# Kernel tuning notes

Hardware: AMD Instinct MI355X
Metric: run time of the kernel (lower is better)

Reference implementation:

```python
import jax, jax.numpy as jnp
import numpy as np

# Module constants (from init_kwargs / derived)
KH, KW = 3, 3
STRIDE = (1, 1)
PAD = (1, 1)
DIL = (1, 1)
N_OFFSET_GRPS = 8  # offset.shape[1] // (2*KH*KW) = 144 // 18
N_WEIGHT_GRPS = 1


def setup_inputs() -> dict:
    key = jax.random.key(0)
    k1, k2, k3, k4, k5 = jax.random.split(key, 5)
    B, C, H, W = 4, 64, 128, 128
    inp = {
        "input": jax.random.normal(k1, (B, C, H, W), dtype=jnp.float32),
        "offset": jax.random.normal(k2, (B, 2 * N_OFFSET_GRPS * KH * KW, H, W), dtype=jnp.float32),
        "mask": jax.random.uniform(k3, (B, N_OFFSET_GRPS * KH * KW, H, W), dtype=jnp.float32),
        "weight": jax.random.normal(k4, (64, C, KH, KW), dtype=jnp.float32) * 0.05,
        "bias": jax.random.normal(k5, (64,), dtype=jnp.float32) * 0.05,
    }
    return inp


def _deform_conv2d(x, offset, mask, weight, bias):
    B, C, H, W = x.shape
    Ho, Wo = offset.shape[2], offset.shape[3]
    G = N_OFFSET_GRPS
    K = KH * KW
    Cg = C // G

    # base (un-deformed) sampling positions per kernel tap and output pixel
    ky, kx = jnp.meshgrid(jnp.arange(KH), jnp.arange(KW), indexing="ij")
    ky = ky.reshape(K)
    kx = kx.reshape(K)
    oy = jnp.arange(Ho) * STRIDE[0] - PAD[0]
    ox = jnp.arange(Wo) * STRIDE[1] - PAD[1]
    base_y = (oy[None, :, None] + (ky * DIL[0])[:, None, None]).astype(x.dtype)  # [K,Ho,1]
    base_x = (ox[None, None, :] + (kx * DIL[1])[:, None, None]).astype(x.dtype)  # [K,1,Wo]

    off = offset.reshape(B, G, K, 2, Ho, Wo)  # [...,0]=dy, [...,1]=dx
    py = base_y[None, None] + off[:, :, :, 0]  # [B,G,K,Ho,Wo]
    px = base_x[None, None] + off[:, :, :, 1]

    y0 = jnp.floor(py)
    x0 = jnp.floor(px)
    ly = py - y0  # fractional parts
    lx = px - x0
    y0i = y0.astype(jnp.int32)
    x0i = x0.astype(jnp.int32)

    xg = x.reshape(B, G, Cg, H * W)  # per-offset-group channel slices

    def corner(yi, xi):
        valid = ((yi >= 0) & (yi < H) & (xi >= 0) & (xi < W)).astype(x.dtype)
        idx = jnp.clip(yi, 0, H - 1) * W + jnp.clip(xi, 0, W - 1)  # [B,G,K,Ho,Wo]
        gather = lambda xbg, ibg: xbg[:, ibg]  # [Cg,H*W],[K,Ho,Wo] -> [Cg,K,Ho,Wo]
        v = jax.vmap(jax.vmap(gather))(xg, idx)  # [B,G,Cg,K,Ho,Wo]
        return v * valid[:, :, None]

    w00 = (1 - ly) * (1 - lx)
    w01 = (1 - ly) * lx
    w10 = ly * (1 - lx)
    w11 = ly * lx
    samp = (corner(y0i, x0i) * w00[:, :, None]
            + corner(y0i, x0i + 1) * w01[:, :, None]
            + corner(y0i + 1, x0i) * w10[:, :, None]
            + corner(y0i + 1, x0i + 1) * w11[:, :, None])  # [B,G,Cg,K,Ho,Wo]

    samp = samp * mask.reshape(B, G, 1, K, Ho, Wo)  # DCNv2 modulation
    col = samp.reshape(B, C, K, Ho, Wo)
    wr = weight.reshape(weight.shape[0], C, K)  # groups == 1
    out = jnp.einsum("ock,bckhw->bohw", wr, col) + bias[None, :, None, None]
    return out


def reference(input, offset, mask, weight, bias):
    return _deform_conv2d(input, offset, mask, weight, bias)
```

## Files before the change

kernel.cpp:

```cpp
#include <hip/hip_runtime.h>

#define HH 128
#define WW 128
#define CC 64
#define CO 64
#define BB 4
#define GG 8
#define CG 8
#define KK 9
#define HW (HH*WW)
#define PXT 16
#define NC 3
#define FRAG 512
#define NPOS (GG*KK*PXT)

typedef __attribute__((ext_vector_type(8))) short short8;
typedef __attribute__((ext_vector_type(4))) float floatx4;

union S8I { short8 s; int i[4]; };

__device__ inline short f2bf(float f) {
    union { float f; unsigned u; } v; v.f = f;
    return (short)((v.u + 0x7FFF + ((v.u >> 16) & 1)) >> 16);
}
__device__ inline unsigned rnd_bf(float f) {
    union { float f; unsigned u; } v; v.f = f;
    return v.u + 0x7FFF + ((v.u >> 16) & 1);
}
__device__ inline float bflo(int e) { union { int i; float f; } u; u.i = e << 16; return u.f; }
__device__ inline float bfhi(int e) { union { int i; float f; } u; u.i = e & 0xffff0000; return u.f; }

__global__ __launch_bounds__(256)
void wt_prepack(const float* __restrict__ wt, short* __restrict__ wf) {
    const int tid = blockIdx.x * 256 + threadIdx.x;
    if (tid >= GG * NC * 4 * FRAG) return;
    const int j  = tid & 7;
    const int L  = (tid >> 3) & 63;
    const int fid = tid >> 9;
    const int ot = fid & 3;
    const int gc = fid >> 2;
    const int c  = gc % 3;
    const int g  = gc / 3;
    const int kp = c * 32 + (L >> 4) * 8 + j;
    const int o  = ot * 16 + (L & 15);
    float val = 0.f;
    if (kp < 72) {
        const int kk = kp >> 3;
        const int cg = kp & 7;
        val = wt[o * 576 + (g * 8 + cg) * 9 + kk];
    }
    wf[tid] = f2bf(val);
}

__global__ __launch_bounds__(256)
void in_transpose(const float* __restrict__ in, short* __restrict__ in_t) {
    const int p = blockIdx.x * 256 + threadIdx.x;
    const int g = blockIdx.y, b = blockIdx.z;
    const float* src = in + (b * CC + g * CG) * HW + p;
    short8 v;
    #pragma unroll
    for (int cg = 0; cg < CG; ++cg) v[cg] = f2bf(src[cg * HW]);
    *(short8*)(in_t + ((b * GG + g) * HW + p) * 8) = v;
}

__global__ __launch_bounds__(256, 4)
void dcn_fused(const short* __restrict__ in_t, const float* __restrict__ off,
               const float* __restrict__ msk, const short* __restrict__ wf,
               const float* __restrict__ bias, float* __restrict__ out)
{
    __shared__ short s_col[GG * NC * FRAG];

    const int pxbase = blockIdx.x * PXT;
    const int ho = blockIdx.y;
    const int b  = blockIdx.z;
    const int t  = threadIdx.x;
    const int w = t >> 6, lane = t & 63;

    float pdy[5], pdx[5], pm[5];
    #pragma unroll
    for (int i = 0; i < 5; ++i) {
        const int pidx = t + i * 256;
        if (pidx < NPOS) {
            const int tc = pidx >> 4;
            const int g  = tc / 9, kk = tc - g * 9;
            const int px = pxbase + (pidx & 15);
            const int base = ho * WW + px;
            const int offc = (b * 144 + g * 18 + kk * 2) * HW + base;
            pdy[i] = off[offc];
            pdx[i] = off[offc + HW];
            pm[i]  = msk[(b * 72 + g * 9 + kk) * HW + base];
        }
    }

    for (int idx = t; idx < 384; idx += 256) {
        const int g = idx / 48, l = (idx - g * 48) + 16;
        ((int4*)s_col)[(g * 3 + 2) * 64 + l] = make_int4(0, 0, 0, 0);
    }

    const int q4 = lane >> 4, n16 = lane & 15;
    floatx4 acc0, acc1;
    #pragma unroll
    for (int r = 0; r < 4; ++r) { acc0[r] = bias[w * 16 + q4 * 4 + r]; acc1[r] = 0.f; }

    const short* inb = in_t + (long)b * GG * HW * 8;
    #pragma unroll
    for (int i = 0; i < 5; ++i) {
        const int pidx = t + i * 256;
        if (pidx < NPOS) {
            const int tc = pidx >> 4;
            const int g  = tc / 9, kk = tc - g * 9;
            const int pl = pidx & 15;
            const int px = pxbase + pl;
            const int ky = kk / 3, kx = kk - ky * 3;

            const float py  = (float)(ho - 1 + ky) + pdy[i];
            const float pxf = (float)(px - 1 + kx) + pdx[i];
            const float y0f = floorf(py), x0f = floorf(pxf);
            const float ly = py - y0f, lx = pxf - x0f;
            const int y0 = (int)y0f, x0 = (int)x0f;
            const int y1 = y0 + 1,  x1 = x0 + 1;

            const float vy0 = (y0 >= 0 && y0 < HH) ? 1.f : 0.f;
            const float vy1 = (y1 >= 0 && y1 < HH) ? 1.f : 0.f;
            const float vx0 = (x0 >= 0 && x0 < WW) ? 1.f : 0.f;
            const float vx1 = (x1 >= 0 && x1 < WW) ? 1.f : 0.f;
            const int y0c = min(max(y0, 0), HH - 1), y1c = min(max(y1, 0), HH - 1);
            const int x0c = min(max(x0, 0), WW - 1), x1c = min(max(x1, 0), WW - 1);

            const float m = pm[i];
            const float w00 = (1.f - ly) * (1.f - lx) * vy0 * vx0 * m;
            const float w01 = (1.f - ly) * lx         * vy0 * vx1 * m;
            const float w10 = ly         * (1.f - lx) * vy1 * vx0 * m;
            const float w11 = ly         * lx         * vy1 * vx1 * m;

            const short* ing = inb + g * (HW * 8);
            S8I u00, u01, u10, u11;
            u00.s = *(const short8*)(ing + (y0c * WW + x0c) * 8);
            u01.s = *(const short8*)(ing + (y0c * WW + x1c) * 8);
            u10.s = *(const short8*)(ing + (y1c * WW + x0c) * 8);
            u11.s = *(const short8*)(ing + (y1c * WW + x1c) * 8);

            S8I res;
            #pragma unroll
            for (int pc = 0; pc < 4; ++pc) {
                const int e00 = u00.i[pc], e01 = u01.i[pc];
                const int e10 = u10.i[pc], e11 = u11.i[pc];
                const float vx_ = w00 * bflo(e00) + w01 * bflo(e01)
                                + w10 * bflo(e10) + w11 * bflo(e11);
                const float vy_ = w00 * bfhi(e00) + w01 * bfhi(e01)
                                + w10 * bfhi(e10) + w11 * bfhi(e11);
                res.i[pc] = (int)__builtin_amdgcn_perm(rnd_bf(vy_), rnd_bf(vx_), 0x07060302u);
            }

            const int c = kk >> 2, q = kk & 3;
            *(short8*)(s_col + ((g * 3 + c) * 64 + q * 16 + pl) * 8) = res.s;
        }
    }

    __syncthreads();

    #pragma unroll
    for (int gc = 0; gc < GG * NC; ++gc) {
        const short8 bfr = *(const short8*)&s_col[(gc * 64 + lane) * 8];
        const short8 afr = *(const short8*)&wf[((gc * 4 + w) * 64 + lane) * 8];
        if (gc & 1) acc1 = __builtin_amdgcn_mfma_f32_16x16x32_bf16(afr, bfr, acc1, 0, 0, 0);
        else        acc0 = __builtin_amdgcn_mfma_f32_16x16x32_bf16(afr, bfr, acc0, 0, 0, 0);
    }

    const int px = pxbase + n16;
    #pragma unroll
    for (int r = 0; r < 4; ++r) {
        const int o = w * 16 + q4 * 4 + r;
        out[((b * CO + o) * HH + ho) * WW + px] = acc0[r] + acc1[r];
    }
}

extern "C" void kernel_launch(void* const* d_in, const int* in_sizes, int n_in,
                              void* d_out, int out_size, void* d_ws, size_t ws_size,
                              hipStream_t stream) {
    const float* in   = (const float*)d_in[0];
    const float* off  = (const float*)d_in[1];
    const float* msk  = (const float*)d_in[2];
    const float* wt   = (const float*)d_in[3];
    const float* bias = (const float*)d_in[4];
    float* out = (float*)d_out;
    short* wf   = (short*)d_ws;
    short* in_t = (short*)d_ws + 49152;

    wt_prepack<<<192, 256, 0, stream>>>(wt, wf);
    in_transpose<<<dim3(HW / 256, GG, BB), 256, 0, stream>>>(in, in_t);

    dim3 grid(WW / PXT, HH, BB);
    dcn_fused<<<grid, 256, 0, stream>>>(in_t, off, msk, wf, bias, out);
}
```

Before: 146.4 us.

## Pack reduction dimension densely, merge prep kernels, raise occupancy bound

Reorders the im2col reduction axis so all 72 group-tap pairs are packed contiguously into 18 MFMA K-chunks instead of 24 per-group padded chunks. This removes zero padding, cuts MFMA count and shared memory, and drops the zero-fill loop. The weight prepack and input transpose are merged into one launch to save a kernel launch. The launch bound raises the waves-per-EU hint to 8, which may force register limits or spills.

```diff
diff --git a/kernel.cpp b/kernel.cpp
--- a/kernel.cpp
+++ b/kernel.cpp
@@ -10,8 +10,7 @@
 #define KK 9
 #define HW (HH*WW)
 #define PXT 16
-#define NC 3
-#define FRAG 512
+#define NCH 18
 #define NPOS (GG*KK*PXT)
 
 typedef __attribute__((ext_vector_type(8))) short short8;
@@ -31,44 +30,42 @@
 __device__ inline float bfhi(int e) { union { int i; float f; } u; u.i = e & 0xffff0000; return u.f; }
 
 __global__ __launch_bounds__(256)
-void wt_prepack(const float* __restrict__ wt, short* __restrict__ wf) {
-    const int tid = blockIdx.x * 256 + threadIdx.x;
-    if (tid >= GG * NC * 4 * FRAG) return;
-    const int j  = tid & 7;
-    const int L  = (tid >> 3) & 63;
-    const int fid = tid >> 9;
-    const int ot = fid & 3;
-    const int gc = fid >> 2;
-    const int c  = gc % 3;
-    const int g  = gc / 3;
-    const int kp = c * 32 + (L >> 4) * 8 + j;
-    const int o  = ot * 16 + (L & 15);
-    float val = 0.f;
-    if (kp < 72) {
-        const int kk = kp >> 3;
-        const int cg = kp & 7;
-        val = wt[o * 576 + (g * 8 + cg) * 9 + kk];
+void prep(const float* __restrict__ wt, const float* __restrict__ in,
+          short* __restrict__ wf, short* __restrict__ in_t) {
+    const int bid = blockIdx.x;
+    if (bid < 144) {
+        const int tid = bid * 256 + threadIdx.x;
+        const int j  = tid & 7;
+        const int L  = (tid >> 3) & 63;
+        const int fid = tid >> 9;
+        const int ot = fid & 3;
+        const int gc = fid >> 2;
+        const int kpp = gc * 32 + (L >> 4) * 8 + j;
+        const int o   = ot * 16 + (L & 15);
+        const int cg  = kpp & 7;
+        const int t72 = kpp >> 3;
+        const int g   = t72 / 9, kk = t72 - g * 9;
+        wf[tid] = f2bf(wt[o * 576 + (g * 8 + cg) * 9 + kk]);
+    } else {
+        const int idx = bid - 144;
+        const int bx = idx & 63;
+        const int g  = (idx >> 6) & 7;
+        const int b  = idx >> 9;
+        const int p  = bx * 256 + threadIdx.x;
+        const float* src = in + (b * CC + g * CG) * HW + p;
+        short8 v;
+        #pragma unroll
+        for (int cg = 0; cg < CG; ++cg) v[cg] = f2bf(src[cg * HW]);
+        *(short8*)(in_t + ((b * GG + g) * HW + p) * 8) = v;
     }
-    wf[tid] = f2bf(val);
 }
 
-__global__ __launch_bounds__(256)
-void in_transpose(const float* __restrict__ in, short* __restrict__ in_t) {
-    const int p = blockIdx.x * 256 + threadIdx.x;
-    const int g = blockIdx.y, b = blockIdx.z;
-    const float* src = in + (b * CC + g * CG) * HW + p;
-    short8 v;
-    #pragma unroll
-    for (int cg = 0; cg < CG; ++cg) v[cg] = f2bf(src[cg * HW]);
-    *(short8*)(in_t + ((b * GG + g) * HW + p) * 8) = v;
-}
-
-__global__ __launch_bounds__(256, 4)
+__global__ __launch_bounds__(256, 8)
 void dcn_fused(const short* __restrict__ in_t, const float* __restrict__ off,
                const float* __restrict__ msk, const short* __restrict__ wf,
                const float* __restrict__ bias, float* __restrict__ out)
 {
-    __shared__ short s_col[GG * NC * FRAG];
+    __shared__ short s_col[NCH * 512];
 
     const int pxbase = blockIdx.x * PXT;
     const int ho = blockIdx.y;
@@ -90,11 +87,6 @@
             pdx[i] = off[offc + HW];
             pm[i]  = msk[(b * 72 + g * 9 + kk) * HW + base];
         }
-    }
-
-    for (int idx = t; idx < 384; idx += 256) {
-        const int g = idx / 48, l = (idx - g * 48) + 16;
-        ((int4*)s_col)[(g * 3 + 2) * 64 + l] = make_int4(0, 0, 0, 0);
     }
 
     const int q4 = lane >> 4, n16 = lane & 15;
@@ -152,15 +144,14 @@
                 res.i[pc] = (int)__builtin_amdgcn_perm(rnd_bf(vy_), rnd_bf(vx_), 0x07060302u);
             }
 
-            const int c = kk >> 2, q = kk & 3;
-            *(short8*)(s_col + ((g * 3 + c) * 64 + q * 16 + pl) * 8) = res.s;
+            *(short8*)(s_col + pidx * 8) = res.s;
         }
     }
 
     __syncthreads();
 
     #pragma unroll
-    for (int gc = 0; gc < GG * NC; ++gc) {
+    for (int gc = 0; gc < NCH; ++gc) {
         const short8 bfr = *(const short8*)&s_col[(gc * 64 + lane) * 8];
         const short8 afr = *(const short8*)&wf[((gc * 4 + w) * 64 + lane) * 8];
         if (gc & 1) acc1 = __builtin_amdgcn_mfma_f32_16x16x32_bf16(afr, bfr, acc1, 0, 0, 0);
@@ -185,10 +176,9 @@
     const float* bias = (const float*)d_in[4];
     float* out = (float*)d_out;
     short* wf   = (short*)d_ws;
-    short* in_t = (short*)d_ws + 49152;
+    short* in_t = (short*)d_ws + 36864;
 
-    wt_prepack<<<192, 256, 0, stream>>>(wt, wf);
-    in_transpose<<<dim3(HW / 256, GG, BB), 256, 0, stream>>>(in, in_t);
+    prep<<<144 + 2048, 256, 0, stream>>>(wt, in, wf, in_t);
 
     dim3 grid(WW / PXT, HH, BB);
     dcn_fused<<<grid, 256, 0, stream>>>(in_t, off, msk, wf, bias, out);
```

Measured after the change: 150.9 us. 3.1% more time.
